# Performance work log

Hardware: AMD Instinct MI355X
Metric: run time of the kernel (lower is better)

The kernel has to match this reference:

```python
import jax, jax.numpy as jnp
import numpy as np
from jax import lax

B, CIN, H, W = 16, 128, 56, 56
COUT, K, STRIDE, PAD, DIL = 256, 3, 1, 1, 1
D = 8  # lattice.d
KE = K * K
M = CIN * KE // D  # sub-vectors per spatial position


def setup_inputs() -> dict:
    key = jax.random.key(0)
    k1, k2, k3 = jax.random.split(key, 3)
    input_encodings = jax.random.normal(k1, (B, CIN, H, W), dtype=jnp.float32)
    weight_encodings = jax.random.normal(k2, (COUT, M, D), dtype=jnp.float32)
    bias = jax.random.normal(k3, (COUT,), dtype=jnp.float32)
    return {"input_encodings": input_encodings,
            "weight_encodings": weight_encodings,
            "bias": bias}


def reference(input_encodings, weight_encodings, bias):
    b, cin, h, w = input_encodings.shape
    cout, m, d = weight_encodings.shape
    h_out = (h + 2 * PAD - DIL * (K - 1) - 1) // STRIDE + 1
    w_out = (w + 2 * PAD - DIL * (K - 1) - 1) // STRIDE + 1
    L = h_out * w_out
    # im2col / unfold: (B, Cin*K*K, Hout, Wout), channel-major (c, kh, kw) ordering
    patches = lax.conv_general_dilated_patches(
        input_encodings, (K, K), (STRIDE, STRIDE), [(PAD, PAD), (PAD, PAD)],
        rhs_dilation=(DIL, DIL))
    # (B, L, M, D): each position split into M lattice-encoded sub-vectors of dim D
    x = patches.reshape(b, cin * K * K, L).transpose(0, 2, 1).reshape(b, L, m, d)
    # two-sided vLUT matrix multiply == sum of per-sub-vector inner products
    out = jnp.einsum('blmd,omd->bol', x, weight_encodings)  # (B, Cout, L)
    out = out.reshape(b, cout, h_out, w_out)
    return out + bias[None, :, None, None]
```

## Files before the change

### kernel.cpp

```cpp
#include <hip/hip_runtime.h>
#include <hip/hip_bf16.h>

#define CIN_   128
#define HW_    56
#define LHW_   3136
#define COUT_  256
#define KTOT_  1152
#define TH_    2
#define SPT_   112
#define NF_    7
#define SCOLS_ 58
#define SPP_   232
#define CSTR_  128

typedef unsigned short u16;
typedef __attribute__((ext_vector_type(8))) short short8v;
typedef __attribute__((ext_vector_type(4))) float f32x4;

__device__ __forceinline__ u16 f2bf(float f) {
  union { float f; unsigned u; } v; v.f = f;
  unsigned u = v.u;
  u += 0x7fffu + ((u >> 16) & 1u);
  return (u16)(u >> 16);
}
__device__ __forceinline__ unsigned pack2(u16 a, u16 b) {
  return (unsigned)a | ((unsigned)b << 16);
}

__global__ void wreorder_kernel(const float* __restrict__ w, u16* __restrict__ wb,
                                u16* __restrict__ zp) {
  if (zp && blockIdx.x == 0 && threadIdx.x < 16) {
    uint4 z; z.x = z.y = z.z = z.w = 0u;
    reinterpret_cast<uint4*>(zp)[threadIdx.x] = z;
  }
  int j = blockIdx.x * 256 + threadIdx.x;
  int c4 = j & 31;
  int o  = (j >> 5) & 255;
  int t  = j >> 13;
  const float* src = w + (size_t)o * KTOT_ + t;
  ushort4 r;
  r.x = f2bf(src[(c4 * 4 + 0) * 9]);
  r.y = f2bf(src[(c4 * 4 + 1) * 9]);
  r.z = f2bf(src[(c4 * 4 + 2) * 9]);
  r.w = f2bf(src[(c4 * 4 + 3) * 9]);
  *reinterpret_cast<ushort4*>(wb + ((size_t)(t * 256 + o) * CSTR_ + c4 * 4)) = r;
}

#define TLDSW_ 136
__global__ __launch_bounds__(256) void nhwc_kernel(
    const float* __restrict__ in, u16* __restrict__ xin) {
  __shared__ u16 ts[64 * TLDSW_];
  const int bp = blockIdx.x;
  const int b = bp / 49;
  const int pos0 = (bp % 49) * 64;
  const int tid = threadIdx.x;
  const float* ib = in + (size_t)b * CIN_ * LHW_ + pos0;
  {
    const int p  = tid & 63;
    const int c0 = (tid >> 6) * 32;
    #pragma unroll
    for (int i = 0; i < 32; ++i)
      ts[p * TLDSW_ + c0 + i] = f2bf(ib[(size_t)(c0 + i) * LHW_ + p]);
  }
  __syncthreads();
  {
    const int p  = tid >> 2;
    const int c0 = (tid & 3) * 32;
    u16* dst = xin + ((size_t)b * LHW_ + pos0 + p) * CIN_ + c0;
    const u16* srcr = &ts[p * TLDSW_ + c0];
    #pragma unroll
    for (int j = 0; j < 4; ++j)
      reinterpret_cast<uint4*>(dst)[j] =
          *reinterpret_cast<const uint4*>(srcr + j * 8);
  }
}

__device__ __forceinline__ void gload_lds16(const void* g, void* l) {
  __builtin_amdgcn_global_load_lds(
      (const __attribute__((address_space(1))) void*)g,
      (__attribute__((address_space(3))) void*)l, 16, 0, 0);
}

__global__ __launch_bounds__(512, 4) void conv3_kernel(
    const u16* __restrict__ xin, const u16* __restrict__ wb,
    const float* __restrict__ bias, const u16* __restrict__ zpage,
    float* __restrict__ out)
{
  __shared__ u16 xs[SPP_ * CSTR_];

  const int tid  = threadIdx.x;
  const int lane = tid & 63;
  const int wid  = tid >> 6;
  const int lr   = lane & 15;
  const int lg   = lane >> 4;

  const int swz = (blockIdx.x & 7) * 56 + (blockIdx.x >> 3);
  const int b   = swz / 28;
  const int ty  = swz % 28;
  const int iy0 = ty * TH_ - 1;

  const u16* xb = xin + (size_t)b * LHW_ * CIN_;

  auto stage_one = [&](int idx) {
    int spp   = idx >> 4;
    int chunk = idx & 15;
    int rr = spp / SCOLS_;
    int cc = spp - rr * SCOLS_;
    int iy = iy0 + rr;
    int ix = cc - 1;
    int sch = chunk ^ (spp & 7);
    const u16* src =
        ((unsigned)iy < (unsigned)HW_ && (unsigned)ix < (unsigned)HW_)
            ? xb + ((size_t)(iy * HW_ + ix) * CIN_ + sch * 8)
            : zpage;
    u16* ldst = xs + (size_t)(idx & ~63) * 8;
    gload_lds16(src, ldst);
  };
  #pragma unroll
  for (int i = 0; i < 7; ++i) stage_one(i * 512 + tid);
  if (tid < 128) stage_one(3584 + tid);

  int spp0[NF_];
  #pragma unroll
  for (int nf = 0; nf < NF_; ++nf) {
    int sp = nf * 16 + lr;
    int r  = (sp >= 56) ? 1 : 0;
    int x  = sp - r * 56;
    spp0[nf] = (r + 1) * SCOLS_ + (x + 1);
  }

  f32x4 acc[2][NF_];
  #pragma unroll
  for (int m = 0; m < 2; ++m)
    #pragma unroll
    for (int nf = 0; nf < NF_; ++nf)
      acc[m][nf] = f32x4{0.f, 0.f, 0.f, 0.f};

  __syncthreads();

  const u16* wt0 = wb + (size_t)(wid * 32 + lr) * CSTR_ + lg * 8;

  #pragma unroll
  for (int t = 0; t < 9; ++t) {
    const int dspp = (t / 3 - 1) * SCOLS_ + (t % 3 - 1);
    const u16* wt = wt0 + (size_t)t * COUT_ * CSTR_;
    #pragma unroll
    for (int c0i = 0; c0i < 4; ++c0i) {
      const int c0 = c0i * 32;
      short8v a0 = *reinterpret_cast<const short8v*>(wt + c0);
      short8v a1 = *reinterpret_cast<const short8v*>(wt + 16 * CSTR_ + c0);
      short8v bv[NF_];
      #pragma unroll
      for (int nf = 0; nf < NF_; ++nf) {
        int spp = spp0[nf] + dspp;
        int off = (spp << 7) + ((c0 + lg * 8) ^ ((spp & 7) << 3));
        bv[nf] = *reinterpret_cast<const short8v*>(&xs[off]);
      }
      #pragma unroll
      for (int nf = 0; nf < NF_; ++nf) {
        acc[0][nf] = __builtin_amdgcn_mfma_f32_16x16x32_bf16(a0, bv[nf], acc[0][nf], 0, 0, 0);
        acc[1][nf] = __builtin_amdgcn_mfma_f32_16x16x32_bf16(a1, bv[nf], acc[1][nf], 0, 0, 0);
      }
    }
  }

  float* ob = out + (size_t)b * COUT_ * LHW_ + ty * SPT_;
  const int obase = wid * 32 + lg * 4;
  #pragma unroll
  for (int m = 0; m < 2; ++m) {
    #pragma unroll
    for (int rr = 0; rr < 4; ++rr) {
      const int o = obase + m * 16 + rr;
      const float bs = bias[o];
      #pragma unroll
      for (int nf = 0; nf < NF_; ++nf)
        ob[(size_t)o * LHW_ + nf * 16 + lr] = acc[m][nf][rr] + bs;
    }
  }
}

__global__ __launch_bounds__(256, 2) void conv2_kernel(
    const float* __restrict__ in, const u16* __restrict__ wb,
    const float* __restrict__ bias, float* __restrict__ out)
{
  __shared__ u16 xs[SPP_ * CSTR_];
  const int tid  = threadIdx.x;
  const int lane = tid & 63;
  const int wid  = tid >> 6;
  const int lr   = lane & 15;
  const int lg   = lane >> 4;
  const int bid = blockIdx.x;
  const int ch  = bid & 1;
  const int ty  = (bid >> 1) % 28;
  const int b   = bid / 56;
  const float* inb = in + (size_t)b * CIN_ * LHW_;
  const int iy0 = ty * TH_ - 1;

  #pragma unroll 1
  for (int i = 0; i < 15; ++i) {
    int idx = i * 256 + tid;
    if (idx < SPP_ * 16) {
      int cg  = idx / SPP_;
      int spp = idx - cg * SPP_;
      int rr  = spp / SCOLS_;
      int cc  = spp - rr * SCOLS_;
      int iy  = iy0 + rr;
      int ix  = cc - 1;
      bool ok = ((unsigned)iy < (unsigned)HW_) && ((unsigned)ix < (unsigned)HW_);
      const float* p = inb + (size_t)cg * 8 * LHW_ + iy * HW_ + ix;
      u16 v[8];
      #pragma unroll
      for (int jj = 0; jj < 8; ++jj)
        v[jj] = f2bf(ok ? p[jj * LHW_] : 0.f);
      uint4 pk;
      pk.x = pack2(v[0], v[1]); pk.y = pack2(v[2], v[3]);
      pk.z = pack2(v[4], v[5]); pk.w = pack2(v[6], v[7]);
      *reinterpret_cast<uint4*>(&xs[spp * CSTR_ + ((cg * 8) ^ ((spp & 7) << 3))]) = pk;
    }
  }
  int spp0[NF_];
  #pragma unroll
  for (int nf = 0; nf < NF_; ++nf) {
    int sp = nf * 16 + lr;
    int r  = (sp >= 56) ? 1 : 0;
    int x  = sp - r * 56;
    spp0[nf] = (r + 1) * SCOLS_ + x + 1;
  }
  f32x4 acc[2][NF_];
  #pragma unroll
  for (int m = 0; m < 2; ++m)
    #pragma unroll
    for (int nf = 0; nf < NF_; ++nf)
      acc[m][nf] = f32x4{0.f, 0.f, 0.f, 0.f};
  __syncthreads();
  const u16* wt0 = wb + (size_t)(ch * 128 + wid * 32 + lr) * CSTR_ + lg * 8;
  #pragma unroll 1
  for (int t = 0; t < 9; ++t) {
    const int dspp = (t / 3 - 1) * SCOLS_ + (t % 3 - 1);
    const u16* wt = wt0 + (size_t)t * 256 * CSTR_;
    #pragma unroll
    for (int c0i = 0; c0i < 4; ++c0i) {
      const int c0 = c0i * 32;
      short8v a0 = *reinterpret_cast<const short8v*>(wt + c0);
      short8v a1 = *reinterpret_cast<const short8v*>(wt + 16 * CSTR_ + c0);
      short8v bv[NF_];
      #pragma unroll
      for (int nf = 0; nf < NF_; ++nf) {
        int spp = spp0[nf] + dspp;
        int off = spp * CSTR_ + ((c0 + lg * 8) ^ ((spp & 7) << 3));
        bv[nf] = *reinterpret_cast<const short8v*>(&xs[off]);
      }
      #pragma unroll
      for (int nf = 0; nf < NF_; ++nf) {
        acc[0][nf] = __builtin_amdgcn_mfma_f32_16x16x32_bf16(a0, bv[nf], acc[0][nf], 0, 0, 0);
        acc[1][nf] = __builtin_amdgcn_mfma_f32_16x16x32_bf16(a1, bv[nf], acc[1][nf], 0, 0, 0);
      }
    }
  }
  float* ob = out + (size_t)b * COUT_ * LHW_ + ty * SPT_;
  const int obase = ch * 128 + wid * 32 + lg * 4;
  #pragma unroll
  for (int m = 0; m < 2; ++m)
    #pragma unroll
    for (int rr = 0; rr < 4; ++rr) {
      const int o = obase + m * 16 + rr;
      const float bs = bias[o];
      #pragma unroll
      for (int nf = 0; nf < NF_; ++nf)
        ob[(size_t)o * LHW_ + nf * 16 + lr] = acc[m][nf][rr] + bs;
    }
}

#define SPT0_  64
#define BK0_   32
#define NKS0_  36
#define LDSW0_ 40
__global__ __launch_bounds__(256, 2) void conv_fb_kernel(
    const float* __restrict__ in, const float* __restrict__ wf,
    const float* __restrict__ bias, float* __restrict__ out)
{
  __shared__ u16 xs[SPT0_ * LDSW0_];
  const int tid = threadIdx.x;
  const int lane = tid & 63;
  const int wid = tid >> 6;
  const int lg = lane >> 4;
  const int lr = lane & 15;
  const int bid = blockIdx.x;
  const int b = bid / 49;
  const int l0 = (bid % 49) * SPT0_;
  const int sp = tid & 63;
  const int qq = tid >> 6;
  const int l = l0 + sp;
  const int y = l / HW_;
  const int x = l - y * HW_;
  const float* inb = in + (size_t)b * CIN_ * LHW_;
  f32x4 acc[4][4];
  #pragma unroll
  for (int i = 0; i < 4; ++i)
    #pragma unroll
    for (int j = 0; j < 4; ++j) acc[i][j] = f32x4{0.f, 0.f, 0.f, 0.f};
  auto stage_load = [&](int ks) -> uint4 {
    int kbase = ks * BK0_ + qq * 8;
    int c = kbase / 9;
    int t = kbase - c * 9;
    u16 v[8];
    #pragma unroll
    for (int j = 0; j < 8; ++j) {
      int dy = (t * 11) >> 5;
      int dx = t - 3 * dy;
      int yy = y + dy - 1, xx = x + dx - 1;
      float f = 0.f;
      if ((unsigned)yy < (unsigned)HW_ && (unsigned)xx < (unsigned)HW_)
        f = inb[(c * HW_ + yy) * HW_ + xx];
      v[j] = f2bf(f);
      ++t; if (t == 9) { t = 0; ++c; }
    }
    uint4 r;
    r.x = pack2(v[0], v[1]); r.y = pack2(v[2], v[3]);
    r.z = pack2(v[4], v[5]); r.w = pack2(v[6], v[7]);
    return r;
  };
  uint4 st = stage_load(0);
  for (int ks = 0; ks < NKS0_; ++ks) {
    __syncthreads();
    *reinterpret_cast<uint4*>(&xs[sp * LDSW0_ + qq * 8]) = st;
    __syncthreads();
    if (ks + 1 < NKS0_) st = stage_load(ks + 1);
    const int k0 = ks * BK0_;
    short8v a[4];
    #pragma unroll
    for (int ai = 0; ai < 4; ++ai) {
      const int o = wid * 64 + ai * 16 + lr;
      const float* p = wf + (size_t)o * KTOT_ + k0 + lg * 8;
      u16 t8[8];
      #pragma unroll
      for (int j = 0; j < 8; ++j) t8[j] = f2bf(p[j]);
      union { uint4 u; short8v s; } cv;
      cv.u.x = pack2(t8[0], t8[1]); cv.u.y = pack2(t8[2], t8[3]);
      cv.u.z = pack2(t8[4], t8[5]); cv.u.w = pack2(t8[6], t8[7]);
      a[ai] = cv.s;
    }
    short8v bv[4];
    #pragma unroll
    for (int sj = 0; sj < 4; ++sj)
      bv[sj] = *reinterpret_cast<const short8v*>(&xs[(sj * 16 + lr) * LDSW0_ + lg * 8]);
    #pragma unroll
    for (int ai = 0; ai < 4; ++ai)
      #pragma unroll
      for (int sj = 0; sj < 4; ++sj)
        acc[ai][sj] = __builtin_amdgcn_mfma_f32_16x16x32_bf16(a[ai], bv[sj], acc[ai][sj], 0, 0, 0);
  }
  float* outb = out + (size_t)b * COUT_ * LHW_ + l0;
  #pragma unroll
  for (int ai = 0; ai < 4; ++ai)
    #pragma unroll
    for (int r = 0; r < 4; ++r) {
      const int o = wid * 64 + ai * 16 + lg * 4 + r;
      const float bvs = bias[o];
      #pragma unroll
      for (int sj = 0; sj < 4; ++sj)
        outb[(size_t)o * LHW_ + sj * 16 + lr] = acc[ai][sj][r] + bvs;
    }
}

extern "C" void kernel_launch(void* const* d_in, const int* in_sizes, int n_in,
                              void* d_out, int out_size, void* d_ws, size_t ws_size,
                              hipStream_t stream) {
  (void)in_sizes; (void)n_in; (void)out_size;
  const float* in   = (const float*)d_in[0];
  const float* w    = (const float*)d_in[1];
  const float* bias = (const float*)d_in[2];
  float* out = (float*)d_out;

  const size_t wbytes  = (size_t)COUT_ * KTOT_ * sizeof(u16);
  const size_t xbytes  = (size_t)16 * LHW_ * CIN_ * sizeof(u16);
  const size_t need    = wbytes + xbytes + 256;

  if (ws_size >= need) {
    u16* wb  = (u16*)d_ws;
    u16* xin = wb + wbytes / 2;
    u16* zp  = xin + xbytes / 2;
    wreorder_kernel<<<dim3(288), dim3(256), 0, stream>>>(w, wb, zp);
    nhwc_kernel<<<dim3(784), dim3(256), 0, stream>>>(in, xin);
    conv3_kernel<<<dim3(448), dim3(512), 0, stream>>>(xin, wb, bias, zp, out);
  } else if (ws_size >= wbytes) {
    u16* wb = (u16*)d_ws;
    wreorder_kernel<<<dim3(288), dim3(256), 0, stream>>>(w, wb, nullptr);
    conv2_kernel<<<dim3(896), dim3(256), 0, stream>>>(in, wb, bias, out);
  } else {
    conv_fb_kernel<<<dim3(784), dim3(256), 0, stream>>>(in, w, bias, out);
  }
}
```

Before: 64.50 us.

## Enlarge conv tile to four rows and software-pipeline MFMA operand loads

```diff
diff --git a/kernel.cpp b/kernel.cpp
--- a/kernel.cpp
+++ b/kernel.cpp
@@ -6,11 +6,11 @@
 #define LHW_   3136
 #define COUT_  256
 #define KTOT_  1152
-#define TH_    2
-#define SPT_   112
+#define TH4_   4
+#define SPB_   224
 #define NF_    7
 #define SCOLS_ 58
-#define SPP_   232
+#define SPP4_  348
 #define CSTR_  128
 
 typedef unsigned short u16;
@@ -27,12 +27,29 @@
   return (unsigned)a | ((unsigned)b << 16);
 }
 
-__global__ void wreorder_kernel(const float* __restrict__ w, u16* __restrict__ wb,
-                                u16* __restrict__ zp) {
-  if (zp && blockIdx.x == 0 && threadIdx.x < 16) {
+__global__ void wreorder2_kernel(const float* __restrict__ w, u16* __restrict__ wb,
+                                 u16* __restrict__ zp) {
+  if (blockIdx.x == 0 && threadIdx.x < 16) {
     uint4 z; z.x = z.y = z.z = z.w = 0u;
     reinterpret_cast<uint4*>(zp)[threadIdx.x] = z;
   }
+  int j = blockIdx.x * 256 + threadIdx.x;
+  int c4 = j & 31;
+  int o  = (j >> 5) & 255;
+  int t  = j >> 13;
+  int c0i = c4 >> 3;
+  int lg  = (c4 >> 1) & 3;
+  size_t slot = ((size_t)(t * 4 + c0i) * 16 + (o >> 4)) * 64 + lg * 16 + (o & 15);
+  const float* src = w + (size_t)o * KTOT_ + t;
+  ushort4 r;
+  r.x = f2bf(src[(c4 * 4 + 0) * 9]);
+  r.y = f2bf(src[(c4 * 4 + 1) * 9]);
+  r.z = f2bf(src[(c4 * 4 + 2) * 9]);
+  r.w = f2bf(src[(c4 * 4 + 3) * 9]);
+  *reinterpret_cast<ushort4*>(wb + slot * 8 + (c4 & 1) * 4) = r;
+}
+
+__global__ void wreorder_kernel(const float* __restrict__ w, u16* __restrict__ wb) {
   int j = blockIdx.x * 256 + threadIdx.x;
   int c4 = j & 31;
   int o  = (j >> 5) & 255;
@@ -81,104 +98,138 @@
       (__attribute__((address_space(3))) void*)l, 16, 0, 0);
 }
 
-__global__ __launch_bounds__(512, 4) void conv3_kernel(
-    const u16* __restrict__ xin, const u16* __restrict__ wb,
+__global__ __launch_bounds__(512, 2) void conv4_kernel(
+    const u16* __restrict__ xin, const u16* __restrict__ wb2,
     const float* __restrict__ bias, const u16* __restrict__ zpage,
     float* __restrict__ out)
 {
-  __shared__ u16 xs[SPP_ * CSTR_];
+  __shared__ u16 xs[SPP4_ * CSTR_];
 
   const int tid  = threadIdx.x;
   const int lane = tid & 63;
   const int wid  = tid >> 6;
+  const int wc   = wid & 3;
+  const int ws   = wid >> 2;
   const int lr   = lane & 15;
   const int lg   = lane >> 4;
-
-  const int swz = (blockIdx.x & 7) * 56 + (blockIdx.x >> 3);
-  const int b   = swz / 28;
-  const int ty  = swz % 28;
-  const int iy0 = ty * TH_ - 1;
+  const int lg8  = lg * 8;
+
+  const int ty = blockIdx.x % 14;
+  const int b  = blockIdx.x / 14;
+  const int iy0 = ty * TH4_ - 1;
 
   const u16* xb = xin + (size_t)b * LHW_ * CIN_;
 
-  auto stage_one = [&](int idx) {
-    int spp   = idx >> 4;
-    int chunk = idx & 15;
-    int rr = spp / SCOLS_;
-    int cc = spp - rr * SCOLS_;
-    int iy = iy0 + rr;
-    int ix = cc - 1;
-    int sch = chunk ^ (spp & 7);
-    const u16* src =
-        ((unsigned)iy < (unsigned)HW_ && (unsigned)ix < (unsigned)HW_)
-            ? xb + ((size_t)(iy * HW_ + ix) * CIN_ + sch * 8)
-            : zpage;
-    u16* ldst = xs + (size_t)(idx & ~63) * 8;
-    gload_lds16(src, ldst);
-  };
-  #pragma unroll
-  for (int i = 0; i < 7; ++i) stage_one(i * 512 + tid);
-  if (tid < 128) stage_one(3584 + tid);
+  #pragma unroll
+  for (int i = 0; i < 11; ++i) {
+    int idx = i * 512 + tid;
+    if (idx < SPP4_ * 16) {
+      int spp   = idx >> 4;
+      int chunk = idx & 15;
+      int rr = spp / SCOLS_;
+      int cc = spp - rr * SCOLS_;
+      int iy = iy0 + rr;
+      int ix = cc - 1;
+      int sch = chunk ^ (spp & 7);
+      const u16* src =
+          ((unsigned)iy < (unsigned)HW_ && (unsigned)ix < (unsigned)HW_)
+              ? xb + ((size_t)(iy * HW_ + ix) * CIN_ + sch * 8)
+              : zpage;
+      u16* ldst = xs + (size_t)(idx & ~63) * 8;
+      gload_lds16(src, ldst);
+    }
+  }
 
   int spp0[NF_];
   #pragma unroll
   for (int nf = 0; nf < NF_; ++nf) {
-    int sp = nf * 16 + lr;
-    int r  = (sp >= 56) ? 1 : 0;
+    int sp = ws * 112 + nf * 16 + lr;
+    int r  = sp / 56;
     int x  = sp - r * 56;
     spp0[nf] = (r + 1) * SCOLS_ + (x + 1);
   }
 
-  f32x4 acc[2][NF_];
-  #pragma unroll
-  for (int m = 0; m < 2; ++m)
+  f32x4 acc[4][NF_];
+  #pragma unroll
+  for (int m = 0; m < 4; ++m)
     #pragma unroll
     for (int nf = 0; nf < NF_; ++nf)
       acc[m][nf] = f32x4{0.f, 0.f, 0.f, 0.f};
 
   __syncthreads();
 
-  const u16* wt0 = wb + (size_t)(wid * 32 + lr) * CSTR_ + lg * 8;
-
-  #pragma unroll
+  const short8v* pA = reinterpret_cast<const short8v*>(wb2);
+
+  auto loadA = [&](int t4c, short8v* dst) {
+    const short8v* p = pA + ((size_t)t4c * 16 + wc * 4) * 64 + lane;
+    #pragma unroll
+    for (int ai = 0; ai < 4; ++ai) dst[ai] = p[ai * 64];
+  };
+  auto loadB = [&](int dspp, int c0, short8v* dst) {
+    #pragma unroll
+    for (int nf = 0; nf < NF_; ++nf) {
+      int spp = spp0[nf] + dspp;
+      int off = (spp << 7) + ((c0 + lg8) ^ ((spp & 7) << 3));
+      dst[nf] = *reinterpret_cast<const short8v*>(&xs[off]);
+    }
+  };
+
+  short8v A0[4], A1[4], B0[NF_], B1[NF_];
+
+#define MFMA_GRP(Ab, Bb)                                                        \
+  {                                                                             \
+    _Pragma("unroll")                                                           \
+    for (int ai = 0; ai < 4; ++ai) {                                            \
+      _Pragma("unroll")                                                         \
+      for (int nf = 0; nf < NF_; ++nf)                                          \
+        acc[ai][nf] = __builtin_amdgcn_mfma_f32_16x16x32_bf16(                  \
+            (Ab)[ai], (Bb)[nf], acc[ai][nf], 0, 0, 0);                          \
+    }                                                                           \
+  }
+
+  loadA(0, A0);
+  loadB(-SCOLS_ - 1, 0, B0);
+
+  #pragma unroll 1
   for (int t = 0; t < 9; ++t) {
-    const int dspp = (t / 3 - 1) * SCOLS_ + (t % 3 - 1);
-    const u16* wt = wt0 + (size_t)t * COUT_ * CSTR_;
-    #pragma unroll
-    for (int c0i = 0; c0i < 4; ++c0i) {
-      const int c0 = c0i * 32;
-      short8v a0 = *reinterpret_cast<const short8v*>(wt + c0);
-      short8v a1 = *reinterpret_cast<const short8v*>(wt + 16 * CSTR_ + c0);
-      short8v bv[NF_];
-      #pragma unroll
-      for (int nf = 0; nf < NF_; ++nf) {
-        int spp = spp0[nf] + dspp;
-        int off = (spp << 7) + ((c0 + lg * 8) ^ ((spp & 7) << 3));
-        bv[nf] = *reinterpret_cast<const short8v*>(&xs[off]);
-      }
-      #pragma unroll
-      for (int nf = 0; nf < NF_; ++nf) {
-        acc[0][nf] = __builtin_amdgcn_mfma_f32_16x16x32_bf16(a0, bv[nf], acc[0][nf], 0, 0, 0);
-        acc[1][nf] = __builtin_amdgcn_mfma_f32_16x16x32_bf16(a1, bv[nf], acc[1][nf], 0, 0, 0);
-      }
-    }
-  }
-
-  float* ob = out + (size_t)b * COUT_ * LHW_ + ty * SPT_;
-  const int obase = wid * 32 + lg * 4;
-  #pragma unroll
-  for (int m = 0; m < 2; ++m) {
+    const int dty  = t / 3;
+    const int dspp = (dty - 1) * SCOLS_ + (t - 3 * dty) - 1;
+    const int t4   = t * 4;
+
+    loadA(t4 + 1, A1); loadB(dspp, 32, B1);
+    MFMA_GRP(A0, B0);
+    loadA(t4 + 2, A0); loadB(dspp, 64, B0);
+    MFMA_GRP(A1, B1);
+    loadA(t4 + 3, A1); loadB(dspp, 96, B1);
+    MFMA_GRP(A0, B0);
+    if (t < 8) {
+      const int tn   = t + 1;
+      const int ndty = tn / 3;
+      const int nds  = (ndty - 1) * SCOLS_ + (tn - 3 * ndty) - 1;
+      loadA(t4 + 4, A0); loadB(nds, 0, B0);
+    }
+    MFMA_GRP(A1, B1);
+  }
+
+  float* ob = out + (size_t)b * COUT_ * LHW_ + ty * SPB_ + ws * 112;
+  const int obase = wc * 64 + lg * 4;
+  #pragma unroll
+  for (int ai = 0; ai < 4; ++ai) {
     #pragma unroll
     for (int rr = 0; rr < 4; ++rr) {
-      const int o = obase + m * 16 + rr;
+      const int o = obase + ai * 16 + rr;
       const float bs = bias[o];
       #pragma unroll
       for (int nf = 0; nf < NF_; ++nf)
-        ob[(size_t)o * LHW_ + nf * 16 + lr] = acc[m][nf][rr] + bs;
-    }
-  }
-}
-
+        ob[(size_t)o * LHW_ + nf * 16 + lr] = acc[ai][nf][rr] + bs;
+    }
+  }
+#undef MFMA_GRP
+}
+
+#define TH_    2
+#define SPT_   112
+#define SPP_   232
 __global__ __launch_bounds__(256, 2) void conv2_kernel(
     const float* __restrict__ in, const u16* __restrict__ wb,
     const float* __restrict__ bias, float* __restrict__ out)
@@ -377,15 +428,15 @@
   const size_t need    = wbytes + xbytes + 256;
 
   if (ws_size >= need) {
-    u16* wb  = (u16*)d_ws;
-    u16* xin = wb + wbytes / 2;
+    u16* wb2 = (u16*)d_ws;
+    u16* xin = wb2 + wbytes / 2;
     u16* zp  = xin + xbytes / 2;
-    wreorder_kernel<<<dim3(288), dim3(256), 0, stream>>>(w, wb, zp);
+    wreorder2_kernel<<<dim3(288), dim3(256), 0, stream>>>(w, wb2, zp);
     nhwc_kernel<<<dim3(784), dim3(256), 0, stream>>>(in, xin);
-    conv3_kernel<<<dim3(448), dim3(512), 0, stream>>>(xin, wb, bias, zp, out);
+    conv4_kernel<<<dim3(224), dim3(512), 0, stream>>>(xin, wb2, bias, zp, out);
   } else if (ws_size >= wbytes) {
     u16* wb = (u16*)d_ws;
-    wreorder_kernel<<<dim3(288), dim3(256), 0, stream>>>(w, wb, nullptr);
+    wreorder_kernel<<<dim3(288), dim3(256), 0, stream>>>(w, wb);
     conv2_kernel<<<dim3(896), dim3(256), 0, stream>>>(in, wb, bias, out);
   } else {
     conv_fb_kernel<<<dim3(784), dim3(256), 0, stream>>>(in, w, bias, out);
```

Result: faster. 61.77 us (-4.2%).
